# Kernel tuning notes

Measured on AMD Instinct MI355X. Metric: run time of the kernel, lower is better.

The kernel has to match this reference:

```python
import jax, jax.numpy as jnp
import numpy as np

EPS = 1e-5      # BatchNorm eps (eval mode, running_mean=0, running_var=1)
SLOPE = 0.2     # LeakyReLU negative slope


def knn_idx(x, k):
    # x: (B, C, N) -> indices of k nearest neighbors (B, N, k)
    xx = jnp.sum(x * x, axis=1)                      # (B, N)
    inner = jnp.einsum('bcn,bcm->bnm', x, x)         # (B, N, N)
    pd = 2.0 * inner - xx[:, :, None] - xx[:, None, :]  # -squared distance
    return jax.lax.top_k(pd, k)[1]


def edge_feature(x, k):
    # x: (B, C, N) -> (B, N, k, 2C) edge features [x_j - x_i, x_i]
    B, C, N = x.shape
    idx = knn_idx(x, k)                              # (B, N, k)
    xt = jnp.transpose(x, (0, 2, 1))                 # (B, N, C)
    feat = jax.vmap(lambda t, i: t[i])(xt, idx)      # (B, N, k, C)
    center = xt[:, :, None, :]                       # (B, N, 1, C)
    return jnp.concatenate(
        [feat - center, jnp.broadcast_to(center, (B, N, k, C))], axis=-1)


def conv_bn_lrelu_max(e, W, g, b):
    # e: (B, N, k, Cin), W: (O, Cin) 1x1 conv; BN eval (mean=0, var=1); max over k
    h = jnp.einsum('bnkc,oc->bnko', e, W)
    scale = g / jnp.sqrt(1.0 + EPS)
    h = h * scale + b
    h = jnp.where(h >= 0, h, SLOPE * h)
    return jnp.transpose(jnp.max(h, axis=2), (0, 2, 1))  # (B, O, N)


def setup_inputs() -> dict:
    key = jax.random.key(0)
    ks = jax.random.split(key, 17)
    B, N, k = 8, 2048, 20
    x = jax.random.normal(ks[0], (B, 3, N), dtype=jnp.float32)
    def w(kk, o, c):
        return jax.random.normal(kk, (o, c), dtype=jnp.float32) * (1.0 / np.sqrt(c))
    W1 = w(ks[1], 64, 6)
    W2 = w(ks[2], 64, 128)
    W3 = w(ks[3], 128, 128)
    W4 = w(ks[4], 256, 256)
    W5 = w(ks[5], 1024, 512)
    def gb(kk, c):
        k1, k2 = jax.random.split(kk)
        g = 0.5 + jax.random.uniform(k1, (c,), dtype=jnp.float32)
        b = 0.1 * jax.random.normal(k2, (c,), dtype=jnp.float32)
        return g, b
    g1, b1 = gb(ks[6], 64)
    g2, b2 = gb(ks[7], 64)
    g3, b3 = gb(ks[8], 128)
    g4, b4 = gb(ks[9], 256)
    g5, b5 = gb(ks[10], 1024)
    return {"x": x, "W1": W1, "W2": W2, "W3": W3, "W4": W4, "W5": W5,
            "g1": g1, "b1": b1, "g2": g2, "b2": b2, "g3": g3, "b3": b3,
            "g4": g4, "b4": b4, "g5": g5, "b5": b5, "k": k}


def reference(x, W1, W2, W3, W4, W5, g1, b1, g2, b2, g3, b3, g4, b4, g5, b5, k):
    h1 = conv_bn_lrelu_max(edge_feature(x, k), W1, g1, b1)    # (B, 64, N)
    h2 = conv_bn_lrelu_max(edge_feature(h1, k), W2, g2, b2)   # (B, 64, N)
    h3 = conv_bn_lrelu_max(edge_feature(h2, k), W3, g3, b3)   # (B, 128, N)
    h4 = conv_bn_lrelu_max(edge_feature(h3, k), W4, g4, b4)   # (B, 256, N)
    cat = jnp.concatenate([h1, h2, h3, h4], axis=1)           # (B, 512, N)
    h = jnp.einsum('bcn,oc->bon', cat, W5)                    # (B, 1024, N)
    h = h * (g5 / jnp.sqrt(1.0 + EPS))[:, None] + b5[:, None]
    h = jnp.where(h >= 0, h, SLOPE * h)
    return jnp.max(h, axis=-1)                                # (B, 1024) maxpool=True
```

## Files before the change

### kernel.cpp

```cpp
#include <hip/hip_runtime.h>
#include <math.h>

#define BB 8
#define NN 2048
#define KK 20

static __device__ __forceinline__ float lrelu(float h) {
    return h >= 0.f ? h : 0.2f * h;
}

__global__ __launch_bounds__(256) void transpose_x(const float* __restrict__ x,
                                                   float* __restrict__ xt) {
    int t = blockIdx.x * 256 + threadIdx.x;
    if (t >= BB * NN) return;
    int b = t / NN, n = t % NN;
    const float* xb = x + (size_t)b * 3 * NN;
    float4 v;
    v.x = xb[n];
    v.y = xb[NN + n];
    v.z = xb[2 * NN + n];
    v.w = 0.f;
    reinterpret_cast<float4*>(xt)[t] = v;
}

__global__ __launch_bounds__(256) void xx_kernel(const float* __restrict__ F, int stride, int off,
                                                 int C, float* __restrict__ xx) {
    int t = blockIdx.x * 256 + threadIdx.x;
    if (t >= BB * NN) return;
    const float* p = F + (size_t)t * stride + off;
    float s = 0.f;
    for (int c = 0; c < C; ++c) { float v = p[c]; s += v * v; }
    xx[t] = s;
}

__global__ __launch_bounds__(256) void wmod_kernel(const float* __restrict__ W, int C, int O,
                                                   float* __restrict__ Wm) {
    int t = blockIdx.x * 256 + threadIdx.x;
    if (t >= 2 * O * C) return;
    int o2 = t / C, c = t % C;
    float v;
    if (o2 < O) v = W[(size_t)o2 * 2 * C + c];
    else {
        int o = o2 - O;
        v = W[(size_t)o * 2 * C + C + c] - W[(size_t)o * 2 * C + c];
    }
    Wm[t] = v;
}

template <int C>
__global__ __launch_bounds__(256) void knn_kernel(const float* __restrict__ F, int stride, int off,
                                                  const float* __restrict__ xx,
                                                  int* __restrict__ idxOut) {
    constexpr int ROWS = 32, TM = 128;
    constexpr int CK = (C >= 64) ? 32 : 4;
    constexpr int SK = (C >= 64) ? 36 : 4;
    constexpr int NKT = (C + CK - 1) / CK;
    constexpr int S4 = SK / 4;
    constexpr int C4 = CK / 4;
    constexpr int PDS = TM + 8;

    __shared__ __align__(16) float As[ROWS * SK];
    __shared__ __align__(16) float Bs[TM * SK];
    __shared__ __align__(16) float pdb[ROWS * PDS];
    __shared__ float xxA[ROWS];
    __shared__ float xxB[TM];

    const int t = threadIdx.x;
    const int b = blockIdx.x / (NN / ROWS);
    const int n0 = (blockIdx.x % (NN / ROWS)) * ROWS;
    const float* Fb = F + (size_t)b * NN * stride + off;
    const float* xxb = xx + (size_t)b * NN;

    unsigned long long tv[KK];
#pragma unroll
    for (int i = 0; i < KK; ++i) tv[i] = 0ull;

    const int rl = t & 3;
    const int cl = t >> 2;
    const int rr = t >> 3;
    const int sub = t & 7;

    if (t < ROWS) xxA[t] = xxb[n0 + t];

    for (int mt = 0; mt < NN / TM; ++mt) {
        const int m0 = mt * TM;
        float acc[8][2];
#pragma unroll
        for (int j = 0; j < 8; ++j) { acc[j][0] = 0.f; acc[j][1] = 0.f; }

        for (int kt = 0; kt < NKT; ++kt) {
            __syncthreads();
            if constexpr (C >= 64) {
                float4* As4w = reinterpret_cast<float4*>(As);
                float4* Bs4w = reinterpret_cast<float4*>(Bs);
                for (int i = t; i < ROWS * S4; i += 256) {
                    int r = i / S4, c4i = i % S4;
                    float4 v = make_float4(0.f, 0.f, 0.f, 0.f);
                    if (c4i < C4)
                        v = *reinterpret_cast<const float4*>(
                            Fb + (size_t)(n0 + r) * stride + kt * CK + 4 * c4i);
                    As4w[i] = v;
                }
                for (int i = t; i < TM * S4; i += 256) {
                    int r = i / S4, c4i = i % S4;
                    float4 v = make_float4(0.f, 0.f, 0.f, 0.f);
                    if (c4i < C4)
                        v = *reinterpret_cast<const float4*>(
                            Fb + (size_t)(m0 + r) * stride + kt * CK + 4 * c4i);
                    Bs4w[i] = v;
                }
            } else {
                if (t < ROWS)
                    reinterpret_cast<float4*>(As)[t] =
                        *reinterpret_cast<const float4*>(Fb + (size_t)(n0 + t) * 4);
                if (t < TM)
                    reinterpret_cast<float4*>(Bs)[t] =
                        *reinterpret_cast<const float4*>(Fb + (size_t)(m0 + t) * 4);
            }
            if (kt == 0) {
                if (t < TM) xxB[t] = xxb[m0 + t];
            }
            __syncthreads();

            const float4* As4 = reinterpret_cast<const float4*>(As);
            const float4* Bs4 = reinterpret_cast<const float4*>(Bs);
#pragma unroll
            for (int c4 = 0; c4 < C4; ++c4) {
                float4 b0 = Bs4[cl * S4 + c4];
                float4 b1 = Bs4[(cl + 64) * S4 + c4];
#pragma unroll
                for (int j = 0; j < 8; ++j) {
                    float4 a = As4[(rl + 4 * j) * S4 + c4];
                    acc[j][0] += a.x * b0.x;
                    acc[j][0] += a.y * b0.y;
                    acc[j][0] += a.z * b0.z;
                    acc[j][0] += a.w * b0.w;
                    acc[j][1] += a.x * b1.x;
                    acc[j][1] += a.y * b1.y;
                    acc[j][1] += a.z * b1.z;
                    acc[j][1] += a.w * b1.w;
                }
            }
        }
#pragma unroll
        for (int j = 0; j < 8; ++j) {
            int r = rl + 4 * j;
            pdb[r * PDS + cl]      = (2.f * acc[j][0] - xxA[r]) - xxB[cl];
            pdb[r * PDS + cl + 64] = (2.f * acc[j][1] - xxA[r]) - xxB[cl + 64];
        }
        __syncthreads();

#pragma unroll
        for (int bb2 = 0; bb2 < 2; ++bb2) {
            unsigned long long kc[8];
#pragma unroll
            for (int jj = 0; jj < 8; ++jj) {
                int ml = sub + 8 * (bb2 * 8 + jj);
                float v = pdb[rr * PDS + ml];
                unsigned int u = __float_as_uint(v);
                unsigned int sv = u ^ (unsigned int)(((int)u >> 31) | 0x80000000);
                kc[jj] = ((unsigned long long)sv << 32) | (unsigned int)(~(m0 + ml));
            }
#pragma unroll
            for (int jj = 0; jj < 8; ++jj) {
                if (kc[jj] > tv[KK - 1]) {
                    unsigned long long c = kc[jj];
#pragma unroll
                    for (int s = KK - 1; s >= 1; --s) {
                        bool shs = c > tv[s];
                        bool shp = c > tv[s - 1];
                        unsigned long long tmp = shp ? tv[s - 1] : c;
                        tv[s] = shs ? tmp : tv[s];
                    }
                    tv[0] = (c > tv[0]) ? c : tv[0];
                }
            }
        }
        __syncthreads();
    }

    int* op = idxOut + ((size_t)b * NN + n0 + rr) * KK;
    for (int s = 0; s < KK; ++s) {
        unsigned long long m = tv[0];
#pragma unroll
        for (int d = 1; d < 8; d <<= 1) {
            unsigned long long o = __shfl_xor(m, d);
            m = (o > m) ? o : m;
        }
        if (sub == 0) op[s] = (int)(~(unsigned int)m);
        bool win = (tv[0] == m);
#pragma unroll
        for (int q = 0; q < KK - 1; ++q) tv[q] = win ? tv[q + 1] : tv[q];
        tv[KK - 1] = win ? 0ull : tv[KK - 1];
    }
}

__global__ __launch_bounds__(256) void gemm_yz(const float* __restrict__ F, int stride, int off,
                                               const float* __restrict__ Wm, int K, int OC,
                                               float* __restrict__ out) {
    __shared__ float As[128 * 36];
    __shared__ float Ws[128 * 36];
    const int t = threadIdx.x;
    const int row0 = blockIdx.x * 128;
    const int col0 = blockIdx.y * 128;
    float acc[8][8];
#pragma unroll
    for (int i = 0; i < 8; ++i)
#pragma unroll
        for (int j = 0; j < 8; ++j) acc[i][j] = 0.f;

    for (int kt = 0; kt < K; kt += 32) {
        __syncthreads();
        for (int i = t; i < 128 * 32; i += 256) {
            int r = i >> 5, c = i & 31;
            int k = kt + c;
            As[r * 36 + c] = (k < K) ? F[(size_t)(row0 + r) * stride + off + k] : 0.f;
            Ws[r * 36 + c] = (k < K) ? Wm[(size_t)(col0 + r) * K + k] : 0.f;
        }
        __syncthreads();
        const int r0 = t & 15, c0 = t >> 4;
        const float4* As4 = reinterpret_cast<const float4*>(As);
        const float4* Ws4 = reinterpret_cast<const float4*>(Ws);
#pragma unroll
        for (int k4 = 0; k4 < 8; ++k4) {
            float4 a[8], w[8];
#pragma unroll
            for (int i = 0; i < 8; ++i) a[i] = As4[(r0 + 16 * i) * 9 + k4];
#pragma unroll
            for (int j = 0; j < 8; ++j) w[j] = Ws4[(c0 + 16 * j) * 9 + k4];
#pragma unroll
            for (int i = 0; i < 8; ++i)
#pragma unroll
                for (int j = 0; j < 8; ++j) {
                    acc[i][j] += a[i].x * w[j].x;
                    acc[i][j] += a[i].y * w[j].y;
                    acc[i][j] += a[i].z * w[j].z;
                    acc[i][j] += a[i].w * w[j].w;
                }
        }
    }
    const int r0 = t & 15, c0 = t >> 4;
#pragma unroll
    for (int i = 0; i < 8; ++i)
#pragma unroll
        for (int j = 0; j < 8; ++j)
            out[(size_t)(row0 + r0 + 16 * i) * OC + col0 + c0 + 16 * j] = acc[i][j];
}

__global__ __launch_bounds__(256) void neighbor_max(const float* __restrict__ yz,
                                                    const int* __restrict__ idx,
                                                    const float* __restrict__ g,
                                                    const float* __restrict__ bia, int O,
                                                    int outOff, float* __restrict__ cat) {
    int t = blockIdx.x * 256 + threadIdx.x;
    int og = O >> 2;
    if (t >= BB * NN * og) return;
    int o4 = t % og;
    int pn = t / og;
    int bbase = (pn >> 11) << 11;
    const int* ip = idx + (size_t)pn * KK;
    int O2 = O * 2;
    float mx = -INFINITY, my = -INFINITY, mz = -INFINITY, mw = -INFINITY;
    for (int j = 0; j < KK; ++j) {
        int nb = ip[j];
        const float4 v =
            *reinterpret_cast<const float4*>(yz + (size_t)(bbase + nb) * O2 + (o4 << 2));
        mx = fmaxf(mx, v.x); my = fmaxf(my, v.y); mz = fmaxf(mz, v.z); mw = fmaxf(mw, v.w);
    }
    const float4 z = *reinterpret_cast<const float4*>(yz + (size_t)pn * O2 + O + (o4 << 2));
    int o = o4 << 2;
    const float inv = 1.f / sqrtf(1.f + 1e-5f);
    float4 r;
    r.x = lrelu((mx + z.x) * (g[o + 0] * inv) + bia[o + 0]);
    r.y = lrelu((my + z.y) * (g[o + 1] * inv) + bia[o + 1]);
    r.z = lrelu((mz + z.z) * (g[o + 2] * inv) + bia[o + 2]);
    r.w = lrelu((mw + z.w) * (g[o + 3] * inv) + bia[o + 3]);
    *reinterpret_cast<float4*>(cat + (size_t)pn * 512 + outOff + o) = r;
}

__global__ __launch_bounds__(256) void final_gemm_max(const float* __restrict__ A,
                                                      const float* __restrict__ W,
                                                      const float* __restrict__ g,
                                                      const float* __restrict__ bia,
                                                      float* __restrict__ partial) {
    __shared__ float As[128 * 36];
    __shared__ float Ws[128 * 36];
    __shared__ float red[16 * 132];
    const int t = threadIdx.x;
    const int row0 = blockIdx.x * 128;
    const int col0 = blockIdx.y * 128;
    float acc[8][8];
#pragma unroll
    for (int i = 0; i < 8; ++i)
#pragma unroll
        for (int j = 0; j < 8; ++j) acc[i][j] = 0.f;

    for (int kt = 0; kt < 512; kt += 32) {
        __syncthreads();
        for (int i = t; i < 128 * 32; i += 256) {
            int r = i >> 5, c = i & 31;
            int k = kt + c;
            As[r * 36 + c] = A[(size_t)(row0 + r) * 512 + k];
            Ws[r * 36 + c] = W[(size_t)(col0 + r) * 512 + k];
        }
        __syncthreads();
        const int r0 = t & 15, c0 = t >> 4;
        const float4* As4 = reinterpret_cast<const float4*>(As);
        const float4* Ws4 = reinterpret_cast<const float4*>(Ws);
#pragma unroll
        for (int k4 = 0; k4 < 8; ++k4) {
            float4 a[8], w[8];
#pragma unroll
            for (int i = 0; i < 8; ++i) a[i] = As4[(r0 + 16 * i) * 9 + k4];
#pragma unroll
            for (int j = 0; j < 8; ++j) w[j] = Ws4[(c0 + 16 * j) * 9 + k4];
#pragma unroll
            for (int i = 0; i < 8; ++i)
#pragma unroll
                for (int j = 0; j < 8; ++j) {
                    acc[i][j] += a[i].x * w[j].x;
                    acc[i][j] += a[i].y * w[j].y;
                    acc[i][j] += a[i].z * w[j].z;
                    acc[i][j] += a[i].w * w[j].w;
                }
        }
    }
    const int r0 = t & 15, c0 = t >> 4;
    const float inv = 1.f / sqrtf(1.f + 1e-5f);
#pragma unroll
    for (int j = 0; j < 8; ++j) {
        int o = col0 + c0 + 16 * j;
        float s = g[o] * inv;
        float bb = bia[o];
        float cm = -INFINITY;
#pragma unroll
        for (int i = 0; i < 8; ++i) {
            float h = acc[i][j] * s + bb;
            h = lrelu(h);
            cm = fmaxf(cm, h);
        }
        red[r0 * 132 + c0 + 16 * j] = cm;
    }
    __syncthreads();
    if (t < 128) {
        float m = -INFINITY;
        for (int q = 0; q < 16; ++q) m = fmaxf(m, red[q * 132 + t]);
        partial[(size_t)blockIdx.x * 1024 + col0 + t] = m;
    }
}

__global__ __launch_bounds__(256) void final_reduce(const float* __restrict__ partial,
                                                    float* __restrict__ out) {
    int t = blockIdx.x * 256 + threadIdx.x;
    if (t >= BB * 1024) return;
    int b = t >> 10, o = t & 1023;
    float m = -INFINITY;
    for (int q = 0; q < 16; ++q) m = fmaxf(m, partial[(size_t)(b * 16 + q) * 1024 + o]);
    out[t] = m;
}

extern "C" void kernel_launch(void* const* d_in, const int* in_sizes, int n_in, void* d_out,
                              int out_size, void* d_ws, size_t ws_size, hipStream_t stream) {
    const float* x  = (const float*)d_in[0];
    const float* W1 = (const float*)d_in[1];
    const float* W2 = (const float*)d_in[2];
    const float* W3 = (const float*)d_in[3];
    const float* W4 = (const float*)d_in[4];
    const float* W5 = (const float*)d_in[5];
    const float* g1 = (const float*)d_in[6];  const float* b1 = (const float*)d_in[7];
    const float* g2 = (const float*)d_in[8];  const float* b2 = (const float*)d_in[9];
    const float* g3 = (const float*)d_in[10]; const float* b3 = (const float*)d_in[11];
    const float* g4 = (const float*)d_in[12]; const float* b4 = (const float*)d_in[13];
    const float* g5 = (const float*)d_in[14]; const float* b5 = (const float*)d_in[15];

    float* ws   = (float*)d_ws;
    float* xt   = ws;
    float* cat  = xt + 65536;
    float* yz   = cat + 8388608;
    float* xxb  = yz + 8388608;
    int*   idxb = (int*)(xxb + 16384);
    float* wmod = (float*)(idxb + 327680);
    float* part = wmod + 65536;

    dim3 blk(256);

    transpose_x<<<dim3(64), blk, 0, stream>>>(x, xt);

    xx_kernel<<<dim3(64), blk, 0, stream>>>(xt, 4, 0, 3, xxb);
    knn_kernel<3><<<dim3(512), blk, 0, stream>>>(xt, 4, 0, xxb, idxb);
    wmod_kernel<<<dim3(2), blk, 0, stream>>>(W1, 3, 64, wmod);
    gemm_yz<<<dim3(128, 1), blk, 0, stream>>>(xt, 4, 0, wmod, 3, 128, yz);
    neighbor_max<<<dim3(1024), blk, 0, stream>>>(yz, idxb, g1, b1, 64, 0, cat);

    xx_kernel<<<dim3(64), blk, 0, stream>>>(cat, 512, 0, 64, xxb);
    knn_kernel<64><<<dim3(512), blk, 0, stream>>>(cat, 512, 0, xxb, idxb);
    wmod_kernel<<<dim3(32), blk, 0, stream>>>(W2, 64, 64, wmod);
    gemm_yz<<<dim3(128, 1), blk, 0, stream>>>(cat, 512, 0, wmod, 64, 128, yz);
    neighbor_max<<<dim3(1024), blk, 0, stream>>>(yz, idxb, g2, b2, 64, 64, cat);

    xx_kernel<<<dim3(64), blk, 0, stream>>>(cat, 512, 64, 64, xxb);
    knn_kernel<64><<<dim3(512), blk, 0, stream>>>(cat, 512, 64, xxb, idxb);
    wmod_kernel<<<dim3(64), blk, 0, stream>>>(W3, 64, 128, wmod);
    gemm_yz<<<dim3(128, 2), blk, 0, stream>>>(cat, 512, 64, wmod, 64, 256, yz);
    neighbor_max<<<dim3(2048), blk, 0, stream>>>(yz, idxb, g3, b3, 128, 128, cat);

    xx_kernel<<<dim3(64), blk, 0, stream>>>(cat, 512, 128, 128, xxb);
    knn_kernel<128><<<dim3(512), blk, 0, stream>>>(cat, 512, 128, xxb, idxb);
    wmod_kernel<<<dim3(256), blk, 0, stream>>>(W4, 128, 256, wmod);
    gemm_yz<<<dim3(128, 4), blk, 0, stream>>>(cat, 512, 128, wmod, 128, 512, yz);
    neighbor_max<<<dim3(4096), blk, 0, stream>>>(yz, idxb, g4, b4, 256, 256, cat);

    final_gemm_max<<<dim3(128, 8), blk, 0, stream>>>(cat, W5, g5, b5, part);
    final_reduce<<<dim3(32), blk, 0, stream>>>(part, (float*)d_out);
}
```

Measured before the change: 1.734 ms.

## Split kNN candidate range across four blocks and merge partial top-k lists

The kNN kernel now divides the candidate points of each row group into four spans, each handled by its own block with a smaller 64-column tile. That quadruples the grid and raises the occupancy hint via launch bounds. Each block writes its packed 64-bit partial top-20 keys into the yz scratch buffer, and a new merge kernel uses 4-lane shuffles to pick the final 20 indices. The aim is to fill more of the GPU during the kNN stages, at the cost of an extra kernel launch and partial-list traffic per layer.

```diff
diff --git a/kernel.cpp b/kernel.cpp
--- a/kernel.cpp
+++ b/kernel.cpp
@@ -48,10 +48,10 @@
 }
 
 template <int C>
-__global__ __launch_bounds__(256) void knn_kernel(const float* __restrict__ F, int stride, int off,
-                                                  const float* __restrict__ xx,
-                                                  int* __restrict__ idxOut) {
-    constexpr int ROWS = 32, TM = 128;
+__global__ __launch_bounds__(256, 4) void knn_kernel(const float* __restrict__ F, int stride,
+                                                     int off, const float* __restrict__ xx,
+                                                     unsigned long long* __restrict__ part) {
+    constexpr int ROWS = 32, TM = 64, NSPLIT = 4, MSPAN = NN / NSPLIT;
     constexpr int CK = (C >= 64) ? 32 : 4;
     constexpr int SK = (C >= 64) ? 36 : 4;
     constexpr int NKT = (C + CK - 1) / CK;
@@ -66,8 +66,10 @@
     __shared__ float xxB[TM];
 
     const int t = threadIdx.x;
-    const int b = blockIdx.x / (NN / ROWS);
-    const int n0 = (blockIdx.x % (NN / ROWS)) * ROWS;
+    const int split = blockIdx.x & (NSPLIT - 1);
+    const int rg = (blockIdx.x >> 2) & 63;
+    const int b = blockIdx.x >> 8;
+    const int n0 = rg * ROWS;
     const float* Fb = F + (size_t)b * NN * stride + off;
     const float* xxb = xx + (size_t)b * NN;
 
@@ -82,11 +84,11 @@
 
     if (t < ROWS) xxA[t] = xxb[n0 + t];
 
-    for (int mt = 0; mt < NN / TM; ++mt) {
-        const int m0 = mt * TM;
-        float acc[8][2];
-#pragma unroll
-        for (int j = 0; j < 8; ++j) { acc[j][0] = 0.f; acc[j][1] = 0.f; }
+    for (int mt = 0; mt < MSPAN / TM; ++mt) {
+        const int m0 = split * MSPAN + mt * TM;
+        float acc[8];
+#pragma unroll
+        for (int j = 0; j < 8; ++j) acc[j] = 0.f;
 
         for (int kt = 0; kt < NKT; ++kt) {
             __syncthreads();
@@ -117,9 +119,7 @@
                     reinterpret_cast<float4*>(Bs)[t] =
                         *reinterpret_cast<const float4*>(Fb + (size_t)(m0 + t) * 4);
             }
-            if (kt == 0) {
-                if (t < TM) xxB[t] = xxb[m0 + t];
-            }
+            if (kt == 0 && t < TM) xxB[t] = xxb[m0 + t];
             __syncthreads();
 
             const float4* As4 = reinterpret_cast<const float4*>(As);
@@ -127,59 +127,50 @@
 #pragma unroll
             for (int c4 = 0; c4 < C4; ++c4) {
                 float4 b0 = Bs4[cl * S4 + c4];
-                float4 b1 = Bs4[(cl + 64) * S4 + c4];
 #pragma unroll
                 for (int j = 0; j < 8; ++j) {
                     float4 a = As4[(rl + 4 * j) * S4 + c4];
-                    acc[j][0] += a.x * b0.x;
-                    acc[j][0] += a.y * b0.y;
-                    acc[j][0] += a.z * b0.z;
-                    acc[j][0] += a.w * b0.w;
-                    acc[j][1] += a.x * b1.x;
-                    acc[j][1] += a.y * b1.y;
-                    acc[j][1] += a.z * b1.z;
-                    acc[j][1] += a.w * b1.w;
+                    acc[j] += a.x * b0.x;
+                    acc[j] += a.y * b0.y;
+                    acc[j] += a.z * b0.z;
+                    acc[j] += a.w * b0.w;
                 }
             }
         }
 #pragma unroll
         for (int j = 0; j < 8; ++j) {
             int r = rl + 4 * j;
-            pdb[r * PDS + cl]      = (2.f * acc[j][0] - xxA[r]) - xxB[cl];
-            pdb[r * PDS + cl + 64] = (2.f * acc[j][1] - xxA[r]) - xxB[cl + 64];
+            pdb[r * PDS + cl] = (2.f * acc[j] - xxA[r]) - xxB[cl];
         }
         __syncthreads();
 
-#pragma unroll
-        for (int bb2 = 0; bb2 < 2; ++bb2) {
-            unsigned long long kc[8];
-#pragma unroll
-            for (int jj = 0; jj < 8; ++jj) {
-                int ml = sub + 8 * (bb2 * 8 + jj);
-                float v = pdb[rr * PDS + ml];
-                unsigned int u = __float_as_uint(v);
-                unsigned int sv = u ^ (unsigned int)(((int)u >> 31) | 0x80000000);
-                kc[jj] = ((unsigned long long)sv << 32) | (unsigned int)(~(m0 + ml));
+        unsigned long long kc[8];
+#pragma unroll
+        for (int jj = 0; jj < 8; ++jj) {
+            int ml = sub + 8 * jj;
+            float v = pdb[rr * PDS + ml];
+            unsigned int u = __float_as_uint(v);
+            unsigned int sv = u ^ (unsigned int)(((int)u >> 31) | 0x80000000);
+            kc[jj] = ((unsigned long long)sv << 32) | (unsigned int)(~(m0 + ml));
+        }
+#pragma unroll
+        for (int jj = 0; jj < 8; ++jj) {
+            if (kc[jj] > tv[KK - 1]) {
+                unsigned long long c = kc[jj];
+#pragma unroll
+                for (int s = KK - 1; s >= 1; --s) {
+                    bool shs = c > tv[s];
+                    bool shp = c > tv[s - 1];
+                    unsigned long long tmp = shp ? tv[s - 1] : c;
+                    tv[s] = shs ? tmp : tv[s];
+                }
+                tv[0] = (c > tv[0]) ? c : tv[0];
             }
-#pragma unroll
-            for (int jj = 0; jj < 8; ++jj) {
-                if (kc[jj] > tv[KK - 1]) {
-                    unsigned long long c = kc[jj];
-#pragma unroll
-                    for (int s = KK - 1; s >= 1; --s) {
-                        bool shs = c > tv[s];
-                        bool shp = c > tv[s - 1];
-                        unsigned long long tmp = shp ? tv[s - 1] : c;
-                        tv[s] = shs ? tmp : tv[s];
-                    }
-                    tv[0] = (c > tv[0]) ? c : tv[0];
-                }
-            }
-        }
-        __syncthreads();
-    }
-
-    int* op = idxOut + ((size_t)b * NN + n0 + rr) * KK;
+        }
+    }
+
+    unsigned long long* op =
+        part + (((size_t)b * NN + n0 + rr) * NSPLIT + split) * KK;
     for (int s = 0; s < KK; ++s) {
         unsigned long long m = tv[0];
 #pragma unroll
@@ -187,11 +178,35 @@
             unsigned long long o = __shfl_xor(m, d);
             m = (o > m) ? o : m;
         }
-        if (sub == 0) op[s] = (int)(~(unsigned int)m);
+        if (sub == 0) op[s] = m;
         bool win = (tv[0] == m);
 #pragma unroll
         for (int q = 0; q < KK - 1; ++q) tv[q] = win ? tv[q + 1] : tv[q];
         tv[KK - 1] = win ? 0ull : tv[KK - 1];
+    }
+}
+
+__global__ __launch_bounds__(256) void knn_merge(const unsigned long long* __restrict__ part,
+                                                 int* __restrict__ idxOut) {
+    int t = blockIdx.x * 256 + threadIdx.x;
+    int q = t & 3, row = t >> 2;
+    if (row >= BB * NN) return;
+    unsigned long long k[KK];
+    const unsigned long long* lp = part + ((size_t)row * 4 + q) * KK;
+#pragma unroll
+    for (int s = 0; s < KK; ++s) k[s] = lp[s];
+    int* op = idxOut + (size_t)row * KK;
+    for (int s = 0; s < KK; ++s) {
+        unsigned long long m = k[0];
+        unsigned long long o1 = __shfl_xor(m, 1);
+        m = (o1 > m) ? o1 : m;
+        unsigned long long o2 = __shfl_xor(m, 2);
+        m = (o2 > m) ? o2 : m;
+        if (q == 0) op[s] = (int)(~(unsigned int)m);
+        bool win = (k[0] == m);
+#pragma unroll
+        for (int qq = 0; qq < KK - 1; ++qq) k[qq] = win ? k[qq + 1] : k[qq];
+        k[KK - 1] = win ? 0ull : k[KK - 1];
     }
 }
 
@@ -381,31 +396,36 @@
     int*   idxb = (int*)(xxb + 16384);
     float* wmod = (float*)(idxb + 327680);
     float* part = wmod + 65536;
+    unsigned long long* knnp = (unsigned long long*)yz;
 
     dim3 blk(256);
 
     transpose_x<<<dim3(64), blk, 0, stream>>>(x, xt);
 
     xx_kernel<<<dim3(64), blk, 0, stream>>>(xt, 4, 0, 3, xxb);
-    knn_kernel<3><<<dim3(512), blk, 0, stream>>>(xt, 4, 0, xxb, idxb);
+    knn_kernel<3><<<dim3(2048), blk, 0, stream>>>(xt, 4, 0, xxb, knnp);
+    knn_merge<<<dim3(256), blk, 0, stream>>>(knnp, idxb);
     wmod_kernel<<<dim3(2), blk, 0, stream>>>(W1, 3, 64, wmod);
     gemm_yz<<<dim3(128, 1), blk, 0, stream>>>(xt, 4, 0, wmod, 3, 128, yz);
     neighbor_max<<<dim3(1024), blk, 0, stream>>>(yz, idxb, g1, b1, 64, 0, cat);
 
     xx_kernel<<<dim3(64), blk, 0, stream>>>(cat, 512, 0, 64, xxb);
-    knn_kernel<64><<<dim3(512), blk, 0, stream>>>(cat, 512, 0, xxb, idxb);
+    knn_kernel<64><<<dim3(2048), blk, 0, stream>>>(cat, 512, 0, xxb, knnp);
+    knn_merge<<<dim3(256), blk, 0, stream>>>(knnp, idxb);
     wmod_kernel<<<dim3(32), blk, 0, stream>>>(W2, 64, 64, wmod);
     gemm_yz<<<dim3(128, 1), blk, 0, stream>>>(cat, 512, 0, wmod, 64, 128, yz);
     neighbor_max<<<dim3(1024), blk, 0, stream>>>(yz, idxb, g2, b2, 64, 64, cat);
 
     xx_kernel<<<dim3(64), blk, 0, stream>>>(cat, 512, 64, 64, xxb);
-    knn_kernel<64><<<dim3(512), blk, 0, stream>>>(cat, 512, 64, xxb, idxb);
+    knn_kernel<64><<<dim3(2048), blk, 0, stream>>>(cat, 512, 64, xxb, knnp);
+    knn_merge<<<dim3(256), blk, 0, stream>>>(knnp, idxb);
     wmod_kernel<<<dim3(64), blk, 0, stream>>>(W3, 64, 128, wmod);
     gemm_yz<<<dim3(128, 2), blk, 0, stream>>>(cat, 512, 64, wmod, 64, 256, yz);
     neighbor_max<<<dim3(2048), blk, 0, stream>>>(yz, idxb, g3, b3, 128, 128, cat);
 
     xx_kernel<<<dim3(64), blk, 0, stream>>>(cat, 512, 128, 128, xxb);
-    knn_kernel<128><<<dim3(512), blk, 0, stream>>>(cat, 512, 128, xxb, idxb);
+    knn_kernel<128><<<dim3(2048), blk, 0, stream>>>(cat, 512, 128, xxb, knnp);
+    knn_merge<<<dim3(256), blk, 0, stream>>>(knnp, idxb);
     wmod_kernel<<<dim3(256), blk, 0, stream>>>(W4, 128, 256, wmod);
     gemm_yz<<<dim3(128, 4), blk, 0, stream>>>(cat, 512, 128, wmod, 128, 512, yz);
     neighbor_max<<<dim3(4096), blk, 0, stream>>>(yz, idxb, g4, b4, 256, 256, cat);
```

Result: faster. 1.495 ms (-13.8%).
